# Performance work log

Hardware: AMD Instinct MI355X
Metric: run time of the kernel (lower is better)

## Reference

```python
import jax, jax.numpy as jnp
import numpy as np

D_MODEL, D_HIDDEN, D_OUTPUT = 512, 1024, 128

def setup_inputs() -> dict:
    key = jax.random.key(0)
    ks = jax.random.split(key, 6)
    enc = jax.random.normal(ks[0], (8, 256, D_MODEL), dtype=jnp.float32)
    dec = jax.random.normal(ks[1], (8, 64, D_MODEL), dtype=jnp.float32)
    s1 = 1.0 / np.sqrt(2 * D_MODEL)
    s2 = 1.0 / np.sqrt(D_HIDDEN)
    W1 = jax.random.uniform(ks[2], (2 * D_MODEL, D_HIDDEN), jnp.float32, -s1, s1)
    b1 = jax.random.uniform(ks[3], (D_HIDDEN,), jnp.float32, -s1, s1)
    W2 = jax.random.uniform(ks[4], (D_HIDDEN, D_OUTPUT), jnp.float32, -s2, s2)
    b2 = jax.random.uniform(ks[5], (D_OUTPUT,), jnp.float32, -s2, s2)
    return {"encoder_state": enc, "decoder_state": dec, "W1": W1, "b1": b1, "W2": W2, "b2": b2}

def reference(encoder_state, decoder_state, W1, b1, W2, b2):
    # Split first linear's weight into encoder/decoder halves: equivalent to
    # concat([enc, dec], -1) @ W1, but avoids materializing the (B,T,U,2d) tensor.
    W_enc, W_dec = W1[:D_MODEL], W1[D_MODEL:]
    enc_proj = jnp.einsum('btd,dh->bth', encoder_state, W_enc)   # (B,T,H)
    dec_proj = jnp.einsum('bud,dh->buh', decoder_state, W_dec)   # (B,U,H)
    hidden = jnp.tanh(enc_proj[:, :, None, :] + dec_proj[:, None, :, :] + b1)  # (B,T,U,H)
    out = jnp.einsum('btuh,ho->btuo', hidden, W2) + b2           # (B,T,U,O)
    return out
```

## Files before the change

### kernel.cpp

```cpp
#include <hip/hip_runtime.h>
#include <hip/hip_bf16.h>


typedef _Float16 f16x8 __attribute__((ext_vector_type(8)));
typedef _Float16 f16x2 __attribute__((ext_vector_type(2)));
typedef float    f32x4 __attribute__((ext_vector_type(4)));

#define C2L 2.8853900817779268f

__device__ __forceinline__ float fast_exp2(float x) { return __builtin_amdgcn_exp2f(x); }

__device__ __forceinline__ f16x2 pk_cvt(float x, float y) {
    auto r = __builtin_amdgcn_cvt_pkrtz(x, y);
    union { decltype(r) a; f16x2 b; } c; c.a = r; return c.b;
}

__device__ __forceinline__ f16x8 tanh8(f16x8 e, f16x8 d) {
    const f16x8 one = {1,1,1,1,1,1,1,1};
    const f16x8 two = {2,2,2,2,2,2,2,2};
    const f16x8 cap = {126,126,126,126,126,126,126,126};
    union { f16x8 v; _Float16 s[8]; } p, r;
    p.v = e * d + one;
    p.v = __builtin_elementwise_min(p.v, cap);
    #pragma unroll
    for (int i = 0; i < 4; ++i) {
        _Float16 q  = p.s[2*i] * p.s[2*i+1];
        _Float16 rq = __builtin_amdgcn_rcph(q);
        r.s[2*i]   = p.s[2*i+1] * rq;
        r.s[2*i+1] = p.s[2*i]   * rq;
    }
    return one - two * r.v;
}

__device__ __forceinline__ void stage16(const void* g, void* l) {
    __builtin_amdgcn_global_load_lds(
        (const __attribute__((address_space(1))) unsigned int*)g,
        (__attribute__((address_space(3))) unsigned int*)l, 16, 0, 0);
}

__global__ __launch_bounds__(1024) void transpose_both(
    const float* __restrict__ W1, const float* __restrict__ W2,
    _Float16* __restrict__ W1T, _Float16* __restrict__ W2T)
{
    __shared__ float tile[32][33];
    int bx = blockIdx.x;
    const float* src; _Float16* dst; int C, c0;
    if (bx < 32) { src = W1; dst = W1T; C = 1024; c0 = bx * 32; }
    else         { src = W2; dst = W2T; C = 128;  c0 = (bx - 32) * 32; }
    int r0 = blockIdx.y * 32;
    int tx = threadIdx.x, ty = threadIdx.y;
    tile[ty][tx] = src[(r0 + ty) * C + (c0 + tx)];
    __syncthreads();
    dst[(size_t)(c0 + ty) * 1024 + (r0 + tx)] = (_Float16)tile[tx][ty];
}

__global__ __launch_bounds__(256) void proj_exp(
    const float* __restrict__ enc,
    const float* __restrict__ dec,
    const _Float16* __restrict__ W1T,
    const float* __restrict__ b1,
    _Float16* __restrict__ Ep,
    _Float16* __restrict__ Dp)
{
    const int K = 512;
    int tid  = threadIdx.x;
    int w    = tid >> 6, lane = tid & 63;
    int quad = lane >> 4, l15 = lane & 15;
    int m_base = blockIdx.y * 64 + w * 16;
    int n_base = blockIdx.x * 64;

    bool is_enc = (m_base < 2048);
    const float* A = is_enc ? (enc + (size_t)(m_base + l15) * K)
                            : (dec + (size_t)(m_base - 2048 + l15) * K);
    int koff = is_enc ? 0 : 512;

    f32x4 acc[4] = {};
    for (int kc = 0; kc < K; kc += 32) {
        int k = kc + quad * 8;
        float4 a_lo = *reinterpret_cast<const float4*>(A + k);
        float4 a_hi = *reinterpret_cast<const float4*>(A + k + 4);
        union { f16x8 v; f16x2 h[4]; } a;
        a.h[0] = pk_cvt(a_lo.x, a_lo.y);
        a.h[1] = pk_cvt(a_lo.z, a_lo.w);
        a.h[2] = pk_cvt(a_hi.x, a_hi.y);
        a.h[3] = pk_cvt(a_hi.z, a_hi.w);
        #pragma unroll
        for (int f = 0; f < 4; ++f) {
            int n = n_base + f * 16 + l15;
            f16x8 b = *reinterpret_cast<const f16x8*>(W1T + n * 1024 + koff + k);
            acc[f] = __builtin_amdgcn_mfma_f32_16x16x32_f16(a.v, b, acc[f], 0, 0, 0);
        }
    }

    #pragma unroll
    for (int f = 0; f < 4; ++f) {
        int col = n_base + f * 16 + l15;
        float bv = is_enc ? b1[col] : 0.0f;
        #pragma unroll
        for (int v = 0; v < 4; ++v) {
            int row = m_base + quad * 4 + v;
            float val = fast_exp2(C2L * (acc[f][v] + bv));
            if (is_enc) Ep[(size_t)row * 1024 + col] = (_Float16)val;
            else        Dp[(size_t)(row - 2048) * 1024 + col] = (_Float16)val;
        }
    }
}

__global__ __launch_bounds__(256, 4) void joint_main(
    const _Float16* __restrict__ Ep,
    const _Float16* __restrict__ Dp,
    const _Float16* __restrict__ W2T,
    const float* __restrict__ b2,
    float* __restrict__ out)
{
    __shared__ _Float16 sB[2][128 * 64];

    int t0 = blockIdx.x * 2, b = blockIdx.y;
    int tid  = threadIdx.x;
    int w    = tid >> 6, lane = tid & 63;
    int quad = lane >> 4, l15 = lane & 15;
    int u0   = w * 16;

    const _Float16* ep0 = Ep + (size_t)(b * 256 + t0) * 1024;
    const _Float16* ep1 = ep0 + 1024;
    const _Float16* dpr = Dp + (size_t)(b * 64 + u0 + l15) * 1024;

    f32x4 acc0[8] = {}, acc1[8] = {};

    #pragma unroll
    for (int i = 0; i < 4; ++i) {
        int c = i * 256 + tid;
        int row = c >> 3, kcs = c & 7;
        stage16(W2T + row * 1024 + ((kcs ^ (row & 7)) << 3),
                &sB[0][(i * 256 + (tid & 0xC0)) * 8]);
    }

    for (int it = 0; it < 16; ++it) {
        __syncthreads();
        if (it < 15) {
            int kb = (it + 1) * 64;
            _Float16* dst = sB[(it + 1) & 1];
            #pragma unroll
            for (int i = 0; i < 4; ++i) {
                int c = i * 256 + tid;
                int row = c >> 3, kcs = c & 7;
                stage16(W2T + row * 1024 + kb + ((kcs ^ (row & 7)) << 3),
                        dst + (i * 256 + (tid & 0xC0)) * 8);
            }
        }
        const _Float16* sb = sB[it & 1];
        #pragma unroll
        for (int ki2 = 0; ki2 < 2; ++ki2) {
            int k = it * 64 + ki2 * 32 + quad * 8;
            f16x8 d8 = *reinterpret_cast<const f16x8*>(dpr + k);
            f16x8 e0 = *reinterpret_cast<const f16x8*>(ep0 + k);
            f16x8 e1 = *reinterpret_cast<const f16x8*>(ep1 + k);
            f16x8 A0 = tanh8(e0, d8);
            f16x8 A1 = tanh8(e1, d8);
            int kc3 = ki2 * 4 + quad;
            int sw  = (kc3 ^ (l15 & 7)) << 3;
            #pragma unroll
            for (int f = 0; f < 8; ++f) {
                f16x8 bb = *reinterpret_cast<const f16x8*>(
                    sb + (f * 16 + l15) * 64 + sw);
                acc0[f] = __builtin_amdgcn_mfma_f32_16x16x32_f16(A0, bb, acc0[f], 0, 0, 0);
                acc1[f] = __builtin_amdgcn_mfma_f32_16x16x32_f16(A1, bb, acc1[f], 0, 0, 0);
            }
        }
    }

    float* o0 = out + (size_t)(b * 256 + t0) * 64 * 128;
    float* o1 = o0 + 64 * 128;
    #pragma unroll
    for (int f = 0; f < 8; ++f) {
        int o = f * 16 + l15;
        float bv = b2[o];
        #pragma unroll
        for (int v = 0; v < 4; ++v) {
            int u = u0 + quad * 4 + v;
            o0[u * 128 + o] = acc0[f][v] + bv;
            o1[u * 128 + o] = acc1[f][v] + bv;
        }
    }
}

extern "C" void kernel_launch(void* const* d_in, const int* in_sizes, int n_in,
                              void* d_out, int out_size, void* d_ws, size_t ws_size,
                              hipStream_t stream) {
    const float* enc = (const float*)d_in[0];
    const float* dec = (const float*)d_in[1];
    const float* W1  = (const float*)d_in[2];
    const float* b1  = (const float*)d_in[3];
    const float* W2  = (const float*)d_in[4];
    const float* b2  = (const float*)d_in[5];
    float* out = (float*)d_out;

    char* ws = (char*)d_ws;
    _Float16* W1T = (_Float16*)(ws);
    _Float16* W2T = (_Float16*)(ws + (2u << 20));
    _Float16* EpP = (_Float16*)(ws + (2u << 20) + (256u << 10));
    _Float16* DpP = (_Float16*)(ws + (6u << 20) + (256u << 10));

    transpose_both<<<dim3(36, 32), dim3(32, 32), 0, stream>>>(W1, W2, W1T, W2T);

    proj_exp<<<dim3(16, 40), 256, 0, stream>>>(enc, dec, W1T, b1, EpP, DpP);

    joint_main<<<dim3(128, 8), 256, 0, stream>>>(EpP, DpP, W2T, b2, out);
}
```

Before: 160.4 us.

## Switch joint GEMM to 32x32x16 MFMA with 4 timesteps per block

The joint kernel now uses 32x32x16 MFMA tiles instead of 16x16x32. Each wave covers 32 decoder positions and 2 timesteps, and each block covers 4 timesteps, so the grid is halved and every staged W2 tile in LDS is reused across twice as many rows. Fewer tanh evaluations are duplicated per output and fewer B-operand LDS reads are issued per FLOP. The cost is larger accumulator register use, with launch bounds relaxed to 2 blocks per CU, and fewer blocks to spread across the CUs.

```diff
diff --git a/kernel.cpp b/kernel.cpp
--- a/kernel.cpp
+++ b/kernel.cpp
@@ -2,9 +2,10 @@
 #include <hip/hip_bf16.h>
 
 
-typedef _Float16 f16x8 __attribute__((ext_vector_type(8)));
-typedef _Float16 f16x2 __attribute__((ext_vector_type(2)));
-typedef float    f32x4 __attribute__((ext_vector_type(4)));
+typedef _Float16 f16x8  __attribute__((ext_vector_type(8)));
+typedef _Float16 f16x2  __attribute__((ext_vector_type(2)));
+typedef float    f32x4  __attribute__((ext_vector_type(4)));
+typedef float    f32x16 __attribute__((ext_vector_type(16)));
 
 #define C2L 2.8853900817779268f
 
@@ -106,7 +107,7 @@
     }
 }
 
-__global__ __launch_bounds__(256, 4) void joint_main(
+__global__ __launch_bounds__(256, 2) void joint_main(
     const _Float16* __restrict__ Ep,
     const _Float16* __restrict__ Dp,
     const _Float16* __restrict__ W2T,
@@ -115,17 +116,18 @@
 {
     __shared__ _Float16 sB[2][128 * 64];
 
-    int t0 = blockIdx.x * 2, b = blockIdx.y;
+    int b    = blockIdx.y;
     int tid  = threadIdx.x;
     int w    = tid >> 6, lane = tid & 63;
-    int quad = lane >> 4, l15 = lane & 15;
-    int u0   = w * 16;
-
-    const _Float16* ep0 = Ep + (size_t)(b * 256 + t0) * 1024;
+    int l31  = lane & 31, hi = lane >> 5;
+    int u0   = (w & 1) * 32;
+    int t0   = blockIdx.x * 4 + (w >> 1) * 2;
+
+    const _Float16* ep0 = Ep + (size_t)(b * 256 + t0) * 1024 + hi * 8;
     const _Float16* ep1 = ep0 + 1024;
-    const _Float16* dpr = Dp + (size_t)(b * 64 + u0 + l15) * 1024;
-
-    f32x4 acc0[8] = {}, acc1[8] = {};
+    const _Float16* dpr = Dp + (size_t)(b * 64 + u0 + l31) * 1024 + hi * 8;
+
+    f32x16 acc0[4] = {}, acc1[4] = {};
 
     #pragma unroll
     for (int i = 0; i < 4; ++i) {
@@ -150,36 +152,36 @@
         }
         const _Float16* sb = sB[it & 1];
         #pragma unroll
-        for (int ki2 = 0; ki2 < 2; ++ki2) {
-            int k = it * 64 + ki2 * 32 + quad * 8;
-            f16x8 d8 = *reinterpret_cast<const f16x8*>(dpr + k);
-            f16x8 e0 = *reinterpret_cast<const f16x8*>(ep0 + k);
-            f16x8 e1 = *reinterpret_cast<const f16x8*>(ep1 + k);
-            f16x8 A0 = tanh8(e0, d8);
-            f16x8 A1 = tanh8(e1, d8);
-            int kc3 = ki2 * 4 + quad;
-            int sw  = (kc3 ^ (l15 & 7)) << 3;
+        for (int k16 = 0; k16 < 4; ++k16) {
+            int kg = it * 64 + k16 * 16;
+            f16x8 dv = *reinterpret_cast<const f16x8*>(dpr + kg);
+            f16x8 e0 = *reinterpret_cast<const f16x8*>(ep0 + kg);
+            f16x8 e1 = *reinterpret_cast<const f16x8*>(ep1 + kg);
+            f16x8 A0 = tanh8(e0, dv);
+            f16x8 A1 = tanh8(e1, dv);
+            int c = k16 * 2 + hi;
+            int sw = (c ^ (l31 & 7)) << 3;
             #pragma unroll
-            for (int f = 0; f < 8; ++f) {
+            for (int of = 0; of < 4; ++of) {
                 f16x8 bb = *reinterpret_cast<const f16x8*>(
-                    sb + (f * 16 + l15) * 64 + sw);
-                acc0[f] = __builtin_amdgcn_mfma_f32_16x16x32_f16(A0, bb, acc0[f], 0, 0, 0);
-                acc1[f] = __builtin_amdgcn_mfma_f32_16x16x32_f16(A1, bb, acc1[f], 0, 0, 0);
+                    sb + (of * 32 + l31) * 64 + sw);
+                acc0[of] = __builtin_amdgcn_mfma_f32_32x32x16_f16(A0, bb, acc0[of], 0, 0, 0);
+                acc1[of] = __builtin_amdgcn_mfma_f32_32x32x16_f16(A1, bb, acc1[of], 0, 0, 0);
             }
         }
     }
 
-    float* o0 = out + (size_t)(b * 256 + t0) * 64 * 128;
+    float* o0 = out + ((size_t)(b * 256 + t0) * 64) * 128;
     float* o1 = o0 + 64 * 128;
     #pragma unroll
-    for (int f = 0; f < 8; ++f) {
-        int o = f * 16 + l15;
+    for (int of = 0; of < 4; ++of) {
+        int o = of * 32 + l31;
         float bv = b2[o];
         #pragma unroll
-        for (int v = 0; v < 4; ++v) {
-            int u = u0 + quad * 4 + v;
-            o0[u * 128 + o] = acc0[f][v] + bv;
-            o1[u * 128 + o] = acc1[f][v] + bv;
+        for (int reg = 0; reg < 16; ++reg) {
+            int u = u0 + (reg & 3) + 8 * (reg >> 2) + 4 * hi;
+            o0[u * 128 + o] = acc0[of][reg] + bv;
+            o1[u * 128 + o] = acc1[of][reg] + bv;
         }
     }
 }
@@ -205,5 +207,5 @@
 
     proj_exp<<<dim3(16, 40), 256, 0, stream>>>(enc, dec, W1T, b1, EpP, DpP);
 
-    joint_main<<<dim3(128, 8), 256, 0, stream>>>(EpP, DpP, W2T, b2, out);
-}
+    joint_main<<<dim3(64, 8), 256, 0, stream>>>(EpP, DpP, W2T, b2, out);
+}
```

After: 165.2 us. +3.0%, slower.
